# Performance work log

Measured on AMD Instinct MI355X. Metric: run time of the kernel, lower is better.

The kernel has to match this reference:

```python
import jax, jax.numpy as jnp
import numpy as np

C = 1.0          # Poincare ball curvature (geoopt PoincareBall default)
EPS = 1e-15      # geoopt clamp epsilon for fp32
FEAT_DIM = 256
NUM_OUTCOME = 128
BATCH = 2048
INIT_EPS = 0.001


def _clamp_abs(x, eps=EPS):
    # keep sign, clamp magnitude away from zero (geoopt clamp_abs)
    s = jnp.where(x >= 0, 1.0, -1.0)
    return s * jnp.maximum(jnp.abs(x), eps)


def mobius_add(x, y, c=C):
    # geoopt _mobius_add with k = -c; x, y broadcastable [..., D]
    k = -c
    x2 = jnp.sum(x * x, axis=-1, keepdims=True)
    y2 = jnp.sum(y * y, axis=-1, keepdims=True)
    xy = jnp.sum(x * y, axis=-1, keepdims=True)
    num = (1.0 - 2.0 * k * xy - k * y2) * x + (1.0 + k * x2) * y
    denom = 1.0 - 2.0 * k * xy + (k * k) * x2 * y2
    return num / jnp.maximum(denom, EPS)


def expmap0(u, c=C):
    # tanh(sqrt(c)||u||) * u / (sqrt(c)||u||)
    sqrt_c = jnp.sqrt(c)
    un = jnp.maximum(jnp.linalg.norm(u, axis=-1, keepdims=True), EPS)
    return jnp.tanh(sqrt_c * un) * u / (sqrt_c * un)


def setup_inputs() -> dict:
    key = jax.random.key(0)
    k1, k2, k3 = jax.random.split(key, 3)
    # input scaled to lie comfortably inside the unit ball
    x = 0.1 * jax.random.normal(k1, (BATCH, FEAT_DIM), dtype=jnp.float32)
    point = INIT_EPS * jax.random.normal(k2, (NUM_OUTCOME, FEAT_DIM), dtype=jnp.float32)
    tangent = INIT_EPS * jax.random.normal(k3, (NUM_OUTCOME, FEAT_DIM), dtype=jnp.float32)
    return {"input": x, "point": point, "tangent": tangent}


def reference(input, point, tangent):
    sqrt_c = jnp.sqrt(jnp.asarray(C, input.dtype))
    x = input.reshape(-1, FEAT_DIM)                    # [B, D]
    p = expmap0(point)                                 # [K, D]
    # vectorized over all K classes at once (replaces python per-class loop)
    diff = mobius_add(-p[None, :, :], x[:, None, :])   # [B, K, D]
    diff_norm2 = jnp.maximum(jnp.sum(diff * diff, axis=-1), EPS)   # [B, K]
    sc_diff_a = jnp.sum(diff * tangent[None, :, :], axis=-1)       # [B, K] signed
    a_norm = jnp.linalg.norm(tangent, axis=-1)                     # [K]
    k = -C
    num = 2.0 * sc_diff_a
    denom = _clamp_abs((1.0 + k * diff_norm2) * a_norm[None, :])
    # arsin_k for k < 0: arcsinh(sqrt(c) * z) / sqrt(c)
    distance = jnp.arcsinh(sqrt_c * (num / denom)) / sqrt_c
    logits = distance * a_norm[None, :]                # scaled=True
    return logits                                      # [B, K]
```

## Files before the change

### kernel.cpp

```cpp
#include <hip/hip_runtime.h>
#include <math.h>


constexpr int D    = 256;
constexpr int Dv   = 64;
constexpr int BT   = 32;
constexpr int KT   = 32;
constexpr int S    = 264;
constexpr float EPS = 1e-15f;

typedef __attribute__((ext_vector_type(8))) short short8;
typedef __attribute__((ext_vector_type(4))) float f32x4;

__device__ __forceinline__ ushort f2bf(float f) {
    uint u = __float_as_uint(f);
    u += 0x7FFFu + ((u >> 16) & 1u);
    return (ushort)(u >> 16);
}

__device__ __forceinline__ float dot4(float4 a, float4 b) {
    return a.x * b.x + a.y * b.y + a.z * b.z + a.w * b.w;
}

__device__ __forceinline__ float epilogue(float s_raw, float t_raw, float U2,
                                          float cc, float P2, float PA, float AN) {
    float s     = cc * s_raw;
    float alpha = 1.f - 2.f * s + U2;
    float beta  = 1.f - P2;
    float gamma = fmaxf(1.f - 2.f * s + P2 * U2, EPS);
    float nn    = alpha * alpha * P2 - 2.f * alpha * beta * s + beta * beta * U2;
    float dn2   = fmaxf(nn / (gamma * gamma), EPS);
    float sc    = (beta * t_raw - alpha * PA) / gamma;
    float draw  = (1.f - dn2) * AN;
    float den   = (draw >= 0.f ? 1.f : -1.f) * fmaxf(fabsf(draw), EPS);
    return asinhf(2.f * sc / den) * AN;
}

__global__ __launch_bounds__(256)
void poincare_mlr_kernel(const float* __restrict__ X,
                         const float* __restrict__ P,
                         const float* __restrict__ A,
                         float* __restrict__ out,
                         int K) {
    __shared__ ushort xs[BT * S];
    __shared__ ushort ps[KT * S];
    __shared__ ushort as_[KT * S];
    __shared__ float U2s[BT];
    __shared__ float kcc[KT], kP2[KT], kPA[KT], kAN[KT];

    const int tid = threadIdx.x;
    const int kb  = blockIdx.x & 3;
    const int bb  = blockIdx.x >> 2;
    const int b0g = bb * BT;
    const int k0g = kb * KT;

    const float4* Xg = (const float4*)(X + (size_t)b0g * D);
    const float4* Pg = (const float4*)(P + (size_t)k0g * D);
    const float4* Ag = (const float4*)(A + (size_t)k0g * D);
    #pragma unroll
    for (int it = 0; it < 8; ++it) {
        int i = tid + 256 * it;
        int r = i >> 6, g = i & 63;
        float4 vx = Xg[r * Dv + g];
        float4 vp = Pg[r * Dv + g];
        float4 va = Ag[r * Dv + g];
        ushort4 bx = make_ushort4(f2bf(vx.x), f2bf(vx.y), f2bf(vx.z), f2bf(vx.w));
        ushort4 bp = make_ushort4(f2bf(vp.x), f2bf(vp.y), f2bf(vp.z), f2bf(vp.w));
        ushort4 ba = make_ushort4(f2bf(va.x), f2bf(va.y), f2bf(va.z), f2bf(va.w));
        *(ushort4*)&xs[r * S + 4 * g]  = bx;
        *(ushort4*)&ps[r * S + 4 * g]  = bp;
        *(ushort4*)&as_[r * S + 4 * g] = ba;
    }

    {
        int r = tid >> 3, g = tid & 7;
        const float4* xr = Xg + (size_t)r * Dv;
        float v = 0.f;
        #pragma unroll
        for (int t = 0; t < 8; ++t) {
            float4 x4 = xr[g + 8 * t];
            v += dot4(x4, x4);
        }
        #pragma unroll
        for (int off = 4; off; off >>= 1) v += __shfl_down(v, off, 8);
        if (g == 0) U2s[r] = v;
    }
    {
        int r = tid >> 3, g = tid & 7;
        const float4* pr = Pg + (size_t)r * Dv;
        const float4* ar = Ag + (size_t)r * Dv;
        float n2 = 0.f, pa = 0.f, a2 = 0.f;
        #pragma unroll
        for (int t = 0; t < 8; ++t) {
            float4 p4 = pr[g + 8 * t];
            float4 a4 = ar[g + 8 * t];
            n2 += dot4(p4, p4);
            pa += dot4(p4, a4);
            a2 += dot4(a4, a4);
        }
        #pragma unroll
        for (int off = 4; off; off >>= 1) {
            n2 += __shfl_down(n2, off, 8);
            pa += __shfl_down(pa, off, 8);
            a2 += __shfl_down(a2, off, 8);
        }
        if (g == 0) {
            float n  = sqrtf(n2);
            float un = fmaxf(n, EPS);
            float cc = tanhf(un) / un;
            kcc[r] = cc;
            kP2[r] = cc * cc * n2;
            kPA[r] = cc * pa;
            kAN[r] = sqrtf(a2);
        }
    }
    __syncthreads();

    const int lane = tid & 63, wv = tid >> 6;
    const int wb = wv >> 1, wk = wv & 1;
    const int m  = lane & 15, kq = lane >> 4;

    const ushort* xb = xs  + (size_t)(wb * 16 + m) * S + kq * 8;
    const ushort* pb = ps  + (size_t)(wk * 16 + m) * S + kq * 8;
    const ushort* ab = as_ + (size_t)(wk * 16 + m) * S + kq * 8;

    f32x4 accS = {0.f, 0.f, 0.f, 0.f};
    f32x4 accT = {0.f, 0.f, 0.f, 0.f};
    #pragma unroll
    for (int st = 0; st < 8; ++st) {
        short8 xa = *(const short8*)(xb + st * 32);
        short8 pf = *(const short8*)(pb + st * 32);
        short8 af = *(const short8*)(ab + st * 32);
        accS = __builtin_amdgcn_mfma_f32_16x16x32_bf16(xa, pf, accS, 0, 0, 0);
        accT = __builtin_amdgcn_mfma_f32_16x16x32_bf16(xa, af, accT, 0, 0, 0);
    }

    const int kloc = wk * 16 + m;
    const float cc = kcc[kloc], P2 = kP2[kloc], PA = kPA[kloc], AN = kAN[kloc];
    const int kg = k0g + kloc;
    #pragma unroll
    for (int j = 0; j < 4; ++j) {
        int rloc = wb * 16 + kq * 4 + j;
        out[(size_t)(b0g + rloc) * K + kg] =
            epilogue(accS[j], accT[j], U2s[rloc], cc, P2, PA, AN);
    }
}

extern "C" void kernel_launch(void* const* d_in, const int* in_sizes, int n_in,
                              void* d_out, int out_size, void* d_ws, size_t ws_size,
                              hipStream_t stream) {
    const float* X = (const float*)d_in[0];
    const float* P = (const float*)d_in[1];
    const float* A = (const float*)d_in[2];
    float* out = (float*)d_out;

    const int B = in_sizes[0] / D;
    const int K = in_sizes[1] / D;

    dim3 grid((B / BT) * (K / KT));
    poincare_mlr_kernel<<<grid, dim3(256), 0, stream>>>(X, P, A, out, K);
}
```

Before: 11.23 us.

## Fuse loads with norm reductions, double block size, use fast intrinsics in epilogue

Merges the bf16 staging pass and the three norm-reduction passes into one pass, so each X/P/A element is read from global memory once instead of twice. Block size goes from 256 to 512 threads. The extra four waves redundantly recompute the MFMA tile and each handles half of the epilogue rows. The epilogue swaps IEEE divides and asinhf for hardware rcp/log/sqrt approximations, and the expmap0 scale uses a Taylor series for small norms. This trades some accuracy and duplicated MFMA work for fewer global loads and more epilogue parallelism.

```diff
diff --git a/kernel.cpp b/kernel.cpp
--- a/kernel.cpp
+++ b/kernel.cpp
@@ -2,11 +2,10 @@
 #include <math.h>
 
 
-constexpr int D    = 256;
-constexpr int Dv   = 64;
-constexpr int BT   = 32;
-constexpr int KT   = 32;
-constexpr int S    = 264;
+constexpr int D   = 256;
+constexpr int BT  = 32;
+constexpr int KT  = 32;
+constexpr int S   = 264;
 constexpr float EPS = 1e-15f;
 
 typedef __attribute__((ext_vector_type(8))) short short8;
@@ -17,7 +16,9 @@
     u += 0x7FFFu + ((u >> 16) & 1u);
     return (ushort)(u >> 16);
 }
-
+__device__ __forceinline__ ushort4 bf4(float4 v) {
+    return make_ushort4(f2bf(v.x), f2bf(v.y), f2bf(v.z), f2bf(v.w));
+}
 __device__ __forceinline__ float dot4(float4 a, float4 b) {
     return a.x * b.x + a.y * b.y + a.z * b.z + a.w * b.w;
 }
@@ -28,15 +29,20 @@
     float alpha = 1.f - 2.f * s + U2;
     float beta  = 1.f - P2;
     float gamma = fmaxf(1.f - 2.f * s + P2 * U2, EPS);
+    float rg    = __builtin_amdgcn_rcpf(gamma);
     float nn    = alpha * alpha * P2 - 2.f * alpha * beta * s + beta * beta * U2;
-    float dn2   = fmaxf(nn / (gamma * gamma), EPS);
-    float sc    = (beta * t_raw - alpha * PA) / gamma;
+    float dn2   = fmaxf(nn * rg * rg, EPS);
+    float sc    = (beta * t_raw - alpha * PA) * rg;
     float draw  = (1.f - dn2) * AN;
     float den   = (draw >= 0.f ? 1.f : -1.f) * fmaxf(fabsf(draw), EPS);
-    return asinhf(2.f * sc / den) * AN;
+    float z     = 2.f * sc * __builtin_amdgcn_rcpf(den);
+    float az    = fabsf(z);
+    float r = __builtin_amdgcn_logf(az + __builtin_amdgcn_sqrtf(__builtin_fmaf(az, az, 1.f)))
+              * 0.6931471805599453f;
+    return (z >= 0.f ? r : -r) * AN;
 }
 
-__global__ __launch_bounds__(256)
+__global__ __launch_bounds__(512, 2)
 void poincare_mlr_kernel(const float* __restrict__ X,
                          const float* __restrict__ P,
                          const float* __restrict__ A,
@@ -54,70 +60,49 @@
     const int b0g = bb * BT;
     const int k0g = kb * KT;
 
-    const float4* Xg = (const float4*)(X + (size_t)b0g * D);
-    const float4* Pg = (const float4*)(P + (size_t)k0g * D);
-    const float4* Ag = (const float4*)(A + (size_t)k0g * D);
-    #pragma unroll
-    for (int it = 0; it < 8; ++it) {
-        int i = tid + 256 * it;
-        int r = i >> 6, g = i & 63;
-        float4 vx = Xg[r * Dv + g];
-        float4 vp = Pg[r * Dv + g];
-        float4 va = Ag[r * Dv + g];
-        ushort4 bx = make_ushort4(f2bf(vx.x), f2bf(vx.y), f2bf(vx.z), f2bf(vx.w));
-        ushort4 bp = make_ushort4(f2bf(vp.x), f2bf(vp.y), f2bf(vp.z), f2bf(vp.w));
-        ushort4 ba = make_ushort4(f2bf(va.x), f2bf(va.y), f2bf(va.z), f2bf(va.w));
-        *(ushort4*)&xs[r * S + 4 * g]  = bx;
-        *(ushort4*)&ps[r * S + 4 * g]  = bp;
-        *(ushort4*)&as_[r * S + 4 * g] = ba;
-    }
-
     {
-        int r = tid >> 3, g = tid & 7;
-        const float4* xr = Xg + (size_t)r * Dv;
-        float v = 0.f;
+        const int rx = tid >> 4, g = tid & 15;
+        const float4* Xr = (const float4*)(X + (size_t)(b0g + rx) * D);
+        const float4* Pr = (const float4*)(P + (size_t)(k0g + rx) * D);
+        const float4* Ar = (const float4*)(A + (size_t)(k0g + rx) * D);
+        float x2 = 0.f, n2 = 0.f, pa = 0.f, a2 = 0.f;
         #pragma unroll
-        for (int t = 0; t < 8; ++t) {
-            float4 x4 = xr[g + 8 * t];
-            v += dot4(x4, x4);
+        for (int t = 0; t < 4; ++t) {
+            const int c = g + 16 * t;
+            float4 vx = Xr[c];
+            float4 vp = Pr[c];
+            float4 va = Ar[c];
+            x2 += dot4(vx, vx);
+            n2 += dot4(vp, vp);
+            pa += dot4(vp, va);
+            a2 += dot4(va, va);
+            *(ushort4*)&xs[rx * S + 4 * c]  = bf4(vx);
+            *(ushort4*)&ps[rx * S + 4 * c]  = bf4(vp);
+            *(ushort4*)&as_[rx * S + 4 * c] = bf4(va);
         }
         #pragma unroll
-        for (int off = 4; off; off >>= 1) v += __shfl_down(v, off, 8);
-        if (g == 0) U2s[r] = v;
-    }
-    {
-        int r = tid >> 3, g = tid & 7;
-        const float4* pr = Pg + (size_t)r * Dv;
-        const float4* ar = Ag + (size_t)r * Dv;
-        float n2 = 0.f, pa = 0.f, a2 = 0.f;
-        #pragma unroll
-        for (int t = 0; t < 8; ++t) {
-            float4 p4 = pr[g + 8 * t];
-            float4 a4 = ar[g + 8 * t];
-            n2 += dot4(p4, p4);
-            pa += dot4(p4, a4);
-            a2 += dot4(a4, a4);
-        }
-        #pragma unroll
-        for (int off = 4; off; off >>= 1) {
-            n2 += __shfl_down(n2, off, 8);
-            pa += __shfl_down(pa, off, 8);
-            a2 += __shfl_down(a2, off, 8);
+        for (int off = 8; off; off >>= 1) {
+            x2 += __shfl_xor(x2, off, 16);
+            n2 += __shfl_xor(n2, off, 16);
+            pa += __shfl_xor(pa, off, 16);
+            a2 += __shfl_xor(a2, off, 16);
         }
         if (g == 0) {
-            float n  = sqrtf(n2);
-            float un = fmaxf(n, EPS);
-            float cc = tanhf(un) / un;
-            kcc[r] = cc;
-            kP2[r] = cc * cc * n2;
-            kPA[r] = cc * pa;
-            kAN[r] = sqrtf(a2);
+            U2s[rx] = x2;
+            float un = fmaxf(__builtin_amdgcn_sqrtf(n2), EPS);
+            float u2 = un * un;
+            float cc = 1.f - u2 * (1.f / 3.f) + u2 * u2 * (2.f / 15.f);
+            if (un > 0.04f) cc = tanhf(un) / un;
+            kcc[rx] = cc;
+            kP2[rx] = cc * cc * n2;
+            kPA[rx] = cc * pa;
+            kAN[rx] = __builtin_amdgcn_sqrtf(a2);
         }
     }
     __syncthreads();
 
     const int lane = tid & 63, wv = tid >> 6;
-    const int wb = wv >> 1, wk = wv & 1;
+    const int wb = wv & 1, wk = (wv >> 1) & 1, jh = wv >> 2;
     const int m  = lane & 15, kq = lane >> 4;
 
     const ushort* xb = xs  + (size_t)(wb * 16 + m) * S + kq * 8;
@@ -135,15 +120,18 @@
         accT = __builtin_amdgcn_mfma_f32_16x16x32_bf16(xa, af, accT, 0, 0, 0);
     }
 
+    const float sA = jh ? accS[2] : accS[0];
+    const float tA = jh ? accT[2] : accT[0];
+    const float sB = jh ? accS[3] : accS[1];
+    const float tB = jh ? accT[3] : accT[1];
+
     const int kloc = wk * 16 + m;
     const float cc = kcc[kloc], P2 = kP2[kloc], PA = kPA[kloc], AN = kAN[kloc];
     const int kg = k0g + kloc;
-    #pragma unroll
-    for (int j = 0; j < 4; ++j) {
-        int rloc = wb * 16 + kq * 4 + j;
-        out[(size_t)(b0g + rloc) * K + kg] =
-            epilogue(accS[j], accT[j], U2s[rloc], cc, P2, PA, AN);
-    }
+    const int r0 = wb * 16 + kq * 4 + jh * 2;
+
+    out[(size_t)(b0g + r0) * K + kg]     = epilogue(sA, tA, U2s[r0],     cc, P2, PA, AN);
+    out[(size_t)(b0g + r0 + 1) * K + kg] = epilogue(sB, tB, U2s[r0 + 1], cc, P2, PA, AN);
 }
 
 extern "C" void kernel_launch(void* const* d_in, const int* in_sizes, int n_in,
@@ -158,5 +146,5 @@
     const int K = in_sizes[1] / D;
 
     dim3 grid((B / BT) * (K / KT));
-    poincare_mlr_kernel<<<grid, dim3(256), 0, stream>>>(X, P, A, out, K);
+    poincare_mlr_kernel<<<grid, dim3(512), 0, stream>>>(X, P, A, out, K);
 }
```

Measured after the change: 10.18 us. 1.1x faster.
